# Performance work log

Measured on AMD Instinct MI355X. Metric: run time of the kernel, lower is better.

Reference implementation:

```python
import jax, jax.numpy as jnp
import numpy as np

NC, NU, K, C, P, O = 20, 16, 128, 2048, 5, 256

def setup_inputs() -> dict:
    key = jax.random.key(0)
    ks = jax.random.split(key, 6)
    s = 0.02  # keep activations well-scaled
    return {
        "topk_feats": jax.random.normal(ks[0], (NC, NU, K, C), jnp.float32),
        "prototypes": jax.random.normal(ks[1], (NC, P, C), jnp.float32),
        "w_inner1": jax.random.normal(ks[2], (O, C), jnp.float32) * s,
        "w_inner_trans": jax.random.normal(ks[3], (C, C), jnp.float32) * s,
        "w_inter1": jax.random.normal(ks[4], (O, C), jnp.float32) * s,
        "w_inter2": jax.random.normal(ks[5], (O, C), jnp.float32) * s,
    }

def reference(topk_feats, prototypes, w_inner1, w_inner_trans, w_inter1, w_inter2):
    scale = 1.0 / jnp.sqrt(jnp.asarray(O, topk_feats.dtype))
    # --- inner (per-group) self-attention, vmapped over (class, unlabel) ---
    # fe: [nc, nu, k, o]
    fe = jnp.einsum("nukc,oc->nuko", topk_feats, w_inner1)
    att = jax.nn.softmax(jnp.einsum("nuko,nulo->nukl", fe, fe) * scale, axis=-1)
    agg = jnp.einsum("nukl,nulc->nukc", att, topk_feats)  # atte @ feat
    feats = topk_feats + jax.nn.relu(jnp.einsum("nukc,dc->nukd", agg, w_inner_trans))
    # --- inter (prototype -> all feats) cross-attention per class ---
    fa = feats.reshape(NC, NU * K, C)  # cat over unlabel dim
    fae = jnp.einsum("nmc,oc->nmo", fa, w_inter1)
    pe = jnp.einsum("npc,oc->npo", prototypes, w_inter2)
    att2 = jax.nn.softmax(jnp.einsum("npo,nmo->npm", pe, fae) * scale, axis=-1)
    un_protos = jnp.einsum("npm,nmc->npc", att2, fa)  # [nc, p, c]
    return un_protos
```

## Files before the change

kernel.cpp:

```cpp
#include <hip/hip_runtime.h>

typedef __attribute__((ext_vector_type(4))) float f32x4;
typedef __attribute__((ext_vector_type(8))) short short8;

#define DEVI static __device__ __forceinline__

DEVI unsigned short f2bf(float f) {
  unsigned int u = __float_as_uint(f);
  u += 0x7FFFu + ((u >> 16) & 1u);
  return (unsigned short)(u >> 16);
}
DEVI float bf2f(unsigned short s) { return __uint_as_float(((unsigned int)s) << 16); }
DEVI unsigned int pack2(float lo, float hi) {
  return ((unsigned int)f2bf(hi) << 16) | (unsigned int)f2bf(lo);
}

#define GL2LDS(gp, lp)                                                        \
  __builtin_amdgcn_global_load_lds(                                           \
      (const __attribute__((address_space(1))) void*)(const void*)(gp),       \
      (__attribute__((address_space(3))) void*)(void*)(lp), 16, 0, 0)

__global__ __launch_bounds__(256) void k_cvt_bf16(const float* __restrict__ src,
                                                  unsigned short* __restrict__ dst, int n4) {
  int i = blockIdx.x * 256 + threadIdx.x;
  if (i < n4) {
    float4 v = ((const float4*)src)[i];
    uint2 o; o.x = pack2(v.x, v.y); o.y = pack2(v.z, v.w);
    ((uint2*)dst)[i] = o;
  }
}

template <bool RES>
__global__ __launch_bounds__(256) void k_gemm_bt(const unsigned short* __restrict__ A,
                                                 const unsigned short* __restrict__ B,
                                                 unsigned short* __restrict__ C,
                                                 const float* __restrict__ resid, int N) {
  constexpr int K = 2048;
  __shared__ unsigned short lA[128 * 64];
  __shared__ unsigned short lB[128 * 64];
  const int tid = threadIdx.x;
  const int lane = tid & 63;
  const int wave = tid >> 6;
  const int wr = wave >> 1, wc = wave & 1;
  const long mBase = (long)blockIdx.y * 128;
  const long nBase = (long)blockIdx.x * 128;

  f32x4 acc[4][4] = {};

  for (int k0 = 0; k0 < K; k0 += 64) {
    __syncthreads();
#pragma unroll
    for (int it = 0; it < 4; it++) {
      int idx = it * 256 + wave * 64 + lane;
      int row = idx >> 3;
      int kc = idx & 7;
      int skc = kc ^ (row & 7);
      const unsigned short* ga = A + (mBase + row) * (long)K + k0 + skc * 8;
      const unsigned short* gb = B + (nBase + row) * (long)K + k0 + skc * 8;
      int lbase = (it * 256 + wave * 64) * 8;
      GL2LDS(ga, &lA[lbase]);
      GL2LDS(gb, &lB[lbase]);
    }
    __syncthreads();
#pragma unroll
    for (int kb = 0; kb < 2; kb++) {
      short8 af[4], bfr[4];
#pragma unroll
      for (int mt = 0; mt < 4; mt++) {
        int row = wr * 64 + mt * 16 + (lane & 15);
        int slot = (kb * 4 + (lane >> 4)) ^ (row & 7);
        af[mt] = *(const short8*)&lA[row * 64 + slot * 8];
      }
#pragma unroll
      for (int nt = 0; nt < 4; nt++) {
        int row = wc * 64 + nt * 16 + (lane & 15);
        int slot = (kb * 4 + (lane >> 4)) ^ (row & 7);
        bfr[nt] = *(const short8*)&lB[row * 64 + slot * 8];
      }
#pragma unroll
      for (int mt = 0; mt < 4; mt++)
#pragma unroll
        for (int nt = 0; nt < 4; nt++)
          acc[mt][nt] = __builtin_amdgcn_mfma_f32_16x16x32_bf16(af[mt], bfr[nt], acc[mt][nt], 0, 0, 0);
    }
  }
#pragma unroll
  for (int mt = 0; mt < 4; mt++) {
#pragma unroll
    for (int nt = 0; nt < 4; nt++) {
#pragma unroll
      for (int j = 0; j < 4; j++) {
        long row = mBase + wr * 64 + mt * 16 + (lane >> 4) * 4 + j;
        long col = nBase + wc * 64 + nt * 16 + (lane & 15);
        float v = acc[mt][nt][j];
        if constexpr (RES) v = resid[row * (long)N + col] + fmaxf(v, 0.0f);
        C[row * (long)N + col] = f2bf(v);
      }
    }
  }
}

template <bool RES>
__global__ __launch_bounds__(512, 2) void k_gemm256(const unsigned short* __restrict__ A,
                                                    const unsigned short* __restrict__ B,
                                                    unsigned short* __restrict__ C,
                                                    const float* __restrict__ resid, int N) {
  constexpr int K = 2048;
  __shared__ unsigned short lA[2][256 * 64];
  __shared__ unsigned short lB[2][256 * 64];
  const int tid = threadIdx.x;
  const int lane = tid & 63;
  const int wave = tid >> 6;
  const int wr = wave >> 2, wc = wave & 3;
  const long mBase = (long)blockIdx.y * 256;
  const long nBase = (long)blockIdx.x * 256;

  f32x4 acc[8][4] = {};

  auto stage = [&](int buf, int k0) {
#pragma unroll
    for (int it = 0; it < 4; it++) {
      int idx = it * 512 + tid;
      int row = idx >> 3, kc = idx & 7;
      int skc = kc ^ (row & 7);
      int lbase = (it * 512 + (tid & ~63)) * 8;
      GL2LDS(A + (mBase + row) * (long)K + k0 + skc * 8, &lA[buf][lbase]);
      GL2LDS(B + (nBase + row) * (long)K + k0 + skc * 8, &lB[buf][lbase]);
    }
  };

  stage(0, 0);
  for (int t = 0; t < 32; t++) {
    const int cur = t & 1;
    if (t < 31) {
      stage(cur ^ 1, (t + 1) * 64);
      asm volatile("s_waitcnt vmcnt(8)" ::: "memory");
    } else {
      asm volatile("s_waitcnt vmcnt(0)" ::: "memory");
    }
    __builtin_amdgcn_s_barrier();
    __builtin_amdgcn_sched_barrier(0);
    const unsigned short* bA = &lA[cur][0];
    const unsigned short* bB = &lB[cur][0];
#pragma unroll
    for (int kb = 0; kb < 2; kb++) {
      short8 af[8], bfr[4];
#pragma unroll
      for (int mt = 0; mt < 8; mt++) {
        int row = wr * 128 + mt * 16 + (lane & 15);
        int slot = (kb * 4 + (lane >> 4)) ^ (row & 7);
        af[mt] = *(const short8*)&bA[row * 64 + slot * 8];
      }
#pragma unroll
      for (int nt = 0; nt < 4; nt++) {
        int row = wc * 64 + nt * 16 + (lane & 15);
        int slot = (kb * 4 + (lane >> 4)) ^ (row & 7);
        bfr[nt] = *(const short8*)&bB[row * 64 + slot * 8];
      }
#pragma unroll
      for (int mt = 0; mt < 8; mt++)
#pragma unroll
        for (int nt = 0; nt < 4; nt++)
          acc[mt][nt] = __builtin_amdgcn_mfma_f32_16x16x32_bf16(af[mt], bfr[nt], acc[mt][nt], 0, 0, 0);
    }
    __builtin_amdgcn_sched_barrier(0);
    __builtin_amdgcn_s_barrier();
  }
#pragma unroll
  for (int mt = 0; mt < 8; mt++) {
#pragma unroll
    for (int nt = 0; nt < 4; nt++) {
#pragma unroll
      for (int j = 0; j < 4; j++) {
        long row = mBase + wr * 128 + mt * 16 + (lane >> 4) * 4 + j;
        long col = nBase + wc * 64 + nt * 16 + (lane & 15);
        float v = acc[mt][nt][j];
        if constexpr (RES) v = resid[row * (long)N + col] + fmaxf(v, 0.0f);
        C[row * (long)N + col] = f2bf(v);
      }
    }
  }
}

__global__ __launch_bounds__(256) void k_attn_inner(const unsigned short* __restrict__ fe,
                                                    const unsigned short* __restrict__ topkb,
                                                    unsigned short* __restrict__ agg) {
  __shared__ unsigned short attb[128 * 136];
  __shared__ unsigned short featT[64 * 128];
  __shared__ float redmax[2 * 128];
  __shared__ float redsum[2 * 128];
  const int tid = threadIdx.x;
  const int lane = tid & 63;
  const int wave = tid >> 6;
  const int wr = wave >> 1, wc = wave & 1;
  const int g = blockIdx.x;
  const unsigned short* feG = fe + (long)g * 128 * 256;

  f32x4 s[4][4] = {};
#pragma unroll
  for (int kb = 0; kb < 8; kb++) {
    short8 af[4], bfr[4];
#pragma unroll
    for (int mt = 0; mt < 4; mt++) {
      int row = wr * 64 + mt * 16 + (lane & 15);
      af[mt] = *(const short8*)(feG + row * 256 + kb * 32 + (lane >> 4) * 8);
    }
#pragma unroll
    for (int nt = 0; nt < 4; nt++) {
      int row = wc * 64 + nt * 16 + (lane & 15);
      bfr[nt] = *(const short8*)(feG + row * 256 + kb * 32 + (lane >> 4) * 8);
    }
#pragma unroll
    for (int mt = 0; mt < 4; mt++)
#pragma unroll
      for (int nt = 0; nt < 4; nt++)
        s[mt][nt] = __builtin_amdgcn_mfma_f32_16x16x32_bf16(af[mt], bfr[nt], s[mt][nt], 0, 0, 0);
  }

  const float cexp = 0.0625f * 1.44269504088896f;
#pragma unroll
  for (int mt = 0; mt < 4; mt++) {
#pragma unroll
    for (int j = 0; j < 4; j++) {
      float m = fmaxf(fmaxf(s[mt][0][j], s[mt][1][j]), fmaxf(s[mt][2][j], s[mt][3][j]));
#pragma unroll
      for (int d = 1; d < 16; d <<= 1) m = fmaxf(m, __shfl_xor(m, d, 64));
      int r = wr * 64 + mt * 16 + (lane >> 4) * 4 + j;
      if ((lane & 15) == 0) redmax[wc * 128 + r] = m;
    }
  }
  __syncthreads();
#pragma unroll
  for (int mt = 0; mt < 4; mt++) {
#pragma unroll
    for (int j = 0; j < 4; j++) {
      int r = wr * 64 + mt * 16 + (lane >> 4) * 4 + j;
      float M = fmaxf(redmax[r], redmax[128 + r]);
      float sm = 0.f;
#pragma unroll
      for (int nt = 0; nt < 4; nt++) {
        float p = exp2f((s[mt][nt][j] - M) * cexp);
        s[mt][nt][j] = p;
        sm += p;
      }
#pragma unroll
      for (int d = 1; d < 16; d <<= 1) sm += __shfl_xor(sm, d, 64);
      if ((lane & 15) == 0) redsum[wc * 128 + r] = sm;
    }
  }
  __syncthreads();
#pragma unroll
  for (int mt = 0; mt < 4; mt++) {
#pragma unroll
    for (int j = 0; j < 4; j++) {
      int r = wr * 64 + mt * 16 + (lane >> 4) * 4 + j;
      float inv = 1.0f / (redsum[r] + redsum[128 + r]);
#pragma unroll
      for (int nt = 0; nt < 4; nt++) {
        int c = wc * 64 + nt * 16 + (lane & 15);
        attb[r * 136 + c] = f2bf(s[mt][nt][j] * inv);
      }
    }
  }

  for (int ch = 0; ch < 32; ch++) {
    __syncthreads();
#pragma unroll
    for (int i = 0; i < 4; i++) {
      int seg = i * 256 + tid;
      int l = seg >> 3, kc = seg & 7;
      const unsigned short* gp = topkb + ((long)g * 128 + l) * 2048 + ch * 64 + kc * 8;
      uint4 w = *(const uint4*)gp;
      unsigned short v[8];
      v[0] = (unsigned short)(w.x & 0xffff); v[1] = (unsigned short)(w.x >> 16);
      v[2] = (unsigned short)(w.y & 0xffff); v[3] = (unsigned short)(w.y >> 16);
      v[4] = (unsigned short)(w.z & 0xffff); v[5] = (unsigned short)(w.z >> 16);
      v[6] = (unsigned short)(w.w & 0xffff); v[7] = (unsigned short)(w.w >> 16);
      int lx = l ^ (kc << 3);
#pragma unroll
      for (int j = 0; j < 8; j++) featT[(kc * 8 + j) * 128 + lx] = v[j];
    }
    __syncthreads();
    f32x4 c[2][4] = {};
#pragma unroll
    for (int kb = 0; kb < 4; kb++) {
      short8 af2[2], bf2v[4];
#pragma unroll
      for (int mt = 0; mt < 2; mt++) {
        int r = wave * 32 + mt * 16 + (lane & 15);
        af2[mt] = *(const short8*)&attb[r * 136 + kb * 32 + (lane >> 4) * 8];
      }
#pragma unroll
      for (int nt = 0; nt < 4; nt++) {
        int cc = nt * 16 + (lane & 15);
        int l0 = (kb * 32 + (lane >> 4) * 8) ^ (((cc >> 3) & 7) << 3);
        bf2v[nt] = *(const short8*)&featT[cc * 128 + l0];
      }
#pragma unroll
      for (int mt = 0; mt < 2; mt++)
#pragma unroll
        for (int nt = 0; nt < 4; nt++)
          c[mt][nt] = __builtin_amdgcn_mfma_f32_16x16x32_bf16(af2[mt], bf2v[nt], c[mt][nt], 0, 0, 0);
    }
#pragma unroll
    for (int mt = 0; mt < 2; mt++)
#pragma unroll
      for (int nt = 0; nt < 4; nt++)
#pragma unroll
        for (int j = 0; j < 4; j++) {
          long row = (long)g * 128 + wave * 32 + mt * 16 + (lane >> 4) * 4 + j;
          int col = ch * 64 + nt * 16 + (lane & 15);
          agg[row * 2048 + col] = f2bf(c[mt][nt][j]);
        }
  }
}

__global__ __launch_bounds__(256) void k_pe(const float* __restrict__ protos,
                                            const float* __restrict__ wi2,
                                            float* __restrict__ pe) {
  int n = blockIdx.x, oc = blockIdx.y, tid = threadIdx.x;
  if (tid < 160) {
    int p = tid >> 5, o = oc * 32 + (tid & 31);
    const float* pr = protos + ((long)n * 5 + p) * 2048;
    const float* wr = wi2 + (long)o * 2048;
    float acc = 0.f;
    for (int cidx = 0; cidx < 2048; cidx += 4) {
      float4 a = *(const float4*)(pr + cidx);
      float4 b = *(const float4*)(wr + cidx);
      acc += a.x * b.x + a.y * b.y + a.z * b.z + a.w * b.w;
    }
    pe[((long)n * 5 + p) * 256 + o] = acc;
  }
}

__global__ __launch_bounds__(256) void k_q(const float* __restrict__ pe,
                                           const float* __restrict__ wi1,
                                           float* __restrict__ q) {
  __shared__ float pel[1280];
  int n = blockIdx.x, cb = blockIdx.y, tid = threadIdx.x;
  for (int i = tid; i < 1280; i += 256) pel[i] = pe[(long)n * 1280 + i];
  __syncthreads();
  int c = cb * 256 + tid;
  float a[5] = {0.f, 0.f, 0.f, 0.f, 0.f};
  for (int o = 0; o < 256; o++) {
    float w = wi1[(long)o * 2048 + c];
#pragma unroll
    for (int p = 0; p < 5; p++) a[p] += pel[p * 256 + o] * w;
  }
#pragma unroll
  for (int p = 0; p < 5; p++) q[((long)n * 5 + p) * 2048 + c] = a[p];
}

__global__ __launch_bounds__(256) void k_lg(const float* __restrict__ q,
                                            const unsigned short* __restrict__ feats,
                                            float* __restrict__ lg) {
  __shared__ float ql[5 * 2048];
  int n = blockIdx.x, mc = blockIdx.y, tid = threadIdx.x;
  const float* qs = q + (long)n * 5 * 2048;
  for (int i = tid; i < 2560; i += 256) ((float4*)ql)[i] = ((const float4*)qs)[i];
  __syncthreads();
  int m = mc * 256 + tid;
  const unsigned short* fr = feats + ((long)n * 2048 + m) * 2048;
  float a[5] = {0.f, 0.f, 0.f, 0.f, 0.f};
  for (int c = 0; c < 2048; c += 8) {
    uint4 w = *(const uint4*)(fr + c);
    float f[8];
    f[0] = bf2f((unsigned short)(w.x & 0xffff)); f[1] = bf2f((unsigned short)(w.x >> 16));
    f[2] = bf2f((unsigned short)(w.y & 0xffff)); f[3] = bf2f((unsigned short)(w.y >> 16));
    f[4] = bf2f((unsigned short)(w.z & 0xffff)); f[5] = bf2f((unsigned short)(w.z >> 16));
    f[6] = bf2f((unsigned short)(w.w & 0xffff)); f[7] = bf2f((unsigned short)(w.w >> 16));
#pragma unroll
    for (int j = 0; j < 8; j++) {
      float fv = f[j];
#pragma unroll
      for (int p = 0; p < 5; p++) a[p] += fv * ql[p * 2048 + c + j];
    }
  }
#pragma unroll
  for (int p = 0; p < 5; p++) lg[((long)n * 5 + p) * 2048 + m] = a[p] * 0.0625f;
}

__global__ __launch_bounds__(256) void k_sm(const float* __restrict__ lg,
                                            float* __restrict__ att2) {
  __shared__ float red[4], red2[4];
  int b = blockIdx.x, tid = threadIdx.x;
  const float* src = lg + (long)b * 2048;
  float v[8];
  float mx = -1e30f;
#pragma unroll
  for (int i = 0; i < 8; i++) { v[i] = src[i * 256 + tid]; mx = fmaxf(mx, v[i]); }
#pragma unroll
  for (int d = 1; d < 64; d <<= 1) mx = fmaxf(mx, __shfl_xor(mx, d, 64));
  if ((tid & 63) == 0) red[tid >> 6] = mx;
  __syncthreads();
  mx = fmaxf(fmaxf(red[0], red[1]), fmaxf(red[2], red[3]));
  float sm = 0.f;
#pragma unroll
  for (int i = 0; i < 8; i++) { v[i] = exp2f((v[i] - mx) * 1.44269504088896f); sm += v[i]; }
#pragma unroll
  for (int d = 1; d < 64; d <<= 1) sm += __shfl_xor(sm, d, 64);
  if ((tid & 63) == 0) red2[tid >> 6] = sm;
  __syncthreads();
  float inv = 1.0f / (red2[0] + red2[1] + red2[2] + red2[3]);
  float* dst = att2 + (long)b * 2048;
#pragma unroll
  for (int i = 0; i < 8; i++) dst[i * 256 + tid] = v[i] * inv;
}

__global__ __launch_bounds__(256) void k_out_part(const float* __restrict__ att2,
                                                  const unsigned short* __restrict__ feats,
                                                  float* __restrict__ partial) {
  __shared__ float a2[5 * 512];
  int n = blockIdx.x, cb = blockIdx.y, ms = blockIdx.z;
  int tid = threadIdx.x;
  const float* src = att2 + (long)n * 5 * 2048 + ms * 512;
  for (int i = tid; i < 640; i += 256) {
    int p = i >> 7, qq = i & 127;
    ((float4*)a2)[i] = *(const float4*)(src + p * 2048 + qq * 4);
  }
  __syncthreads();
  int c0 = cb * 1024 + tid * 4;
  const unsigned short* fp = feats + ((long)n * 2048 + ms * 512) * 2048 + c0;
  float acc[5][4] = {};
  for (int m = 0; m < 512; m++) {
    uint2 w = *(const uint2*)(fp + (long)m * 2048);
    float f0 = bf2f((unsigned short)(w.x & 0xffff));
    float f1 = bf2f((unsigned short)(w.x >> 16));
    float f2 = bf2f((unsigned short)(w.y & 0xffff));
    float f3 = bf2f((unsigned short)(w.y >> 16));
#pragma unroll
    for (int p = 0; p < 5; p++) {
      float a = a2[p * 512 + m];
      acc[p][0] += a * f0; acc[p][1] += a * f1; acc[p][2] += a * f2; acc[p][3] += a * f3;
    }
  }
  float* pp = partial + ((long)ms * 100 + (long)n * 5) * 2048;
#pragma unroll
  for (int p = 0; p < 5; p++) {
    float4 o; o.x = acc[p][0]; o.y = acc[p][1]; o.z = acc[p][2]; o.w = acc[p][3];
    *(float4*)(pp + p * 2048 + c0) = o;
  }
}

__global__ __launch_bounds__(256) void k_out_red(const float* __restrict__ partial,
                                                 float* __restrict__ outp) {
  int i = blockIdx.x * 256 + threadIdx.x;
  const f32x4* P = (const f32x4*)partial;
  f32x4 s = P[i] + P[51200 + i] + P[2 * 51200 + i] + P[3 * 51200 + i];
  ((f32x4*)outp)[i] = s;
}

extern "C" void kernel_launch(void* const* d_in, const int* in_sizes, int n_in,
                              void* d_out, int out_size, void* d_ws, size_t ws_size,
                              hipStream_t stream) {
  const float* topk = (const float*)d_in[0];
  const float* protos = (const float*)d_in[1];
  const float* w1 = (const float*)d_in[2];
  const float* wt = (const float*)d_in[3];
  const float* wi1 = (const float*)d_in[4];
  const float* wi2 = (const float*)d_in[5];
  float* outp = (float*)d_out;

  char* ws = (char*)d_ws;
  size_t off = 0;
  auto alloc = [&](size_t bytes) -> void* {
    void* p = ws + off;
    off += (bytes + 255) & ~(size_t)255;
    return p;
  };
  unsigned short* w1b = (unsigned short*)alloc((size_t)256 * 2048 * 2);
  unsigned short* wtb = (unsigned short*)alloc((size_t)2048 * 2048 * 2);
  unsigned short* topkb = (unsigned short*)alloc((size_t)40960 * 2048 * 2);
  unsigned short* fe = (unsigned short*)alloc((size_t)40960 * 256 * 2);
  unsigned short* agg = (unsigned short*)alloc((size_t)40960 * 2048 * 2);
  float* pe = (float*)alloc((size_t)20 * 5 * 256 * 4);
  float* q = (float*)alloc((size_t)20 * 5 * 2048 * 4);
  float* lg = (float*)alloc((size_t)20 * 5 * 2048 * 4);
  float* att2 = (float*)alloc((size_t)20 * 5 * 2048 * 4);
  float* partial = (float*)alloc((size_t)4 * 20 * 5 * 2048 * 4);
  unsigned short* feats = topkb;

  k_cvt_bf16<<<512, 256, 0, stream>>>(w1, w1b, 131072);
  k_cvt_bf16<<<4096, 256, 0, stream>>>(wt, wtb, 1048576);
  k_cvt_bf16<<<81920, 256, 0, stream>>>(topk, topkb, 20971520);

  k_gemm_bt<false><<<dim3(2, 320), 256, 0, stream>>>(topkb, w1b, fe, nullptr, 256);
  k_attn_inner<<<320, 256, 0, stream>>>(fe, topkb, agg);
  k_gemm256<true><<<dim3(8, 160), 512, 0, stream>>>(agg, wtb, feats, topk, 2048);
  k_pe<<<dim3(20, 8), 256, 0, stream>>>(protos, wi2, pe);
  k_q<<<dim3(20, 8), 256, 0, stream>>>(pe, wi1, q);
  k_lg<<<dim3(20, 8), 256, 0, stream>>>(q, feats, lg);
  k_sm<<<100, 256, 0, stream>>>(lg, att2);
  k_out_part<<<dim3(20, 2, 4), 256, 0, stream>>>(att2, feats, partial);
  k_out_red<<<200, 256, 0, stream>>>(partial, outp);
}
```

Measured before the change: 1.041 ms.

## Double-buffer small GEMM, swizzle block order, split tail kernels for more parallelism

The 128-tile GEMM gets double-buffered LDS staging with explicit vmcnt waits so loads overlap MFMA work. Both GEMMs also remap block indices in an XCD-aware swizzle to improve L2 locality. The logits kernel is split along channels into two partial outputs that the softmax kernel sums, and the output kernel uses narrower per-thread column chunks with twice as many blocks. The aim is to raise occupancy in the tail kernels, which launch too few blocks to fill the GPU. The cost is more LDS, extra partial buffers and slightly more memory traffic.

```diff
diff --git a/kernel.cpp b/kernel.cpp
--- a/kernel.cpp
+++ b/kernel.cpp
@@ -36,32 +36,46 @@
                                                  unsigned short* __restrict__ C,
                                                  const float* __restrict__ resid, int N) {
   constexpr int K = 2048;
-  __shared__ unsigned short lA[128 * 64];
-  __shared__ unsigned short lB[128 * 64];
+  __shared__ unsigned short lA[2][128 * 64];
+  __shared__ unsigned short lB[2][128 * 64];
   const int tid = threadIdx.x;
   const int lane = tid & 63;
   const int wave = tid >> 6;
   const int wr = wave >> 1, wc = wave & 1;
-  const long mBase = (long)blockIdx.y * 128;
-  const long nBase = (long)blockIdx.x * 128;
+  const int nx = gridDim.x;
+  const int lin = blockIdx.y * nx + blockIdx.x;
+  const int cpx = (nx * gridDim.y) >> 3;
+  const int swz = (lin & 7) * cpx + (lin >> 3);
+  const long mBase = (long)(swz / nx) * 128;
+  const long nBase = (long)(swz % nx) * 128;
 
   f32x4 acc[4][4] = {};
 
-  for (int k0 = 0; k0 < K; k0 += 64) {
-    __syncthreads();
+  auto stage = [&](int buf, int k0) {
 #pragma unroll
     for (int it = 0; it < 4; it++) {
-      int idx = it * 256 + wave * 64 + lane;
-      int row = idx >> 3;
-      int kc = idx & 7;
+      int idx = it * 256 + tid;
+      int row = idx >> 3, kc = idx & 7;
       int skc = kc ^ (row & 7);
-      const unsigned short* ga = A + (mBase + row) * (long)K + k0 + skc * 8;
-      const unsigned short* gb = B + (nBase + row) * (long)K + k0 + skc * 8;
-      int lbase = (it * 256 + wave * 64) * 8;
-      GL2LDS(ga, &lA[lbase]);
-      GL2LDS(gb, &lB[lbase]);
-    }
-    __syncthreads();
+      int lbase = (it * 256 + (tid & ~63)) * 8;
+      GL2LDS(A + (mBase + row) * (long)K + k0 + skc * 8, &lA[buf][lbase]);
+      GL2LDS(B + (nBase + row) * (long)K + k0 + skc * 8, &lB[buf][lbase]);
+    }
+  };
+
+  stage(0, 0);
+  for (int t = 0; t < 32; t++) {
+    const int cur = t & 1;
+    if (t < 31) {
+      stage(cur ^ 1, (t + 1) * 64);
+      asm volatile("s_waitcnt vmcnt(8)" ::: "memory");
+    } else {
+      asm volatile("s_waitcnt vmcnt(0)" ::: "memory");
+    }
+    __builtin_amdgcn_s_barrier();
+    __builtin_amdgcn_sched_barrier(0);
+    const unsigned short* bA = &lA[cur][0];
+    const unsigned short* bB = &lB[cur][0];
 #pragma unroll
     for (int kb = 0; kb < 2; kb++) {
       short8 af[4], bfr[4];
@@ -69,13 +83,13 @@
       for (int mt = 0; mt < 4; mt++) {
         int row = wr * 64 + mt * 16 + (lane & 15);
         int slot = (kb * 4 + (lane >> 4)) ^ (row & 7);
-        af[mt] = *(const short8*)&lA[row * 64 + slot * 8];
+        af[mt] = *(const short8*)&bA[row * 64 + slot * 8];
       }
 #pragma unroll
       for (int nt = 0; nt < 4; nt++) {
         int row = wc * 64 + nt * 16 + (lane & 15);
         int slot = (kb * 4 + (lane >> 4)) ^ (row & 7);
-        bfr[nt] = *(const short8*)&lB[row * 64 + slot * 8];
+        bfr[nt] = *(const short8*)&bB[row * 64 + slot * 8];
       }
 #pragma unroll
       for (int mt = 0; mt < 4; mt++)
@@ -83,6 +97,8 @@
         for (int nt = 0; nt < 4; nt++)
           acc[mt][nt] = __builtin_amdgcn_mfma_f32_16x16x32_bf16(af[mt], bfr[nt], acc[mt][nt], 0, 0, 0);
     }
+    __builtin_amdgcn_sched_barrier(0);
+    __builtin_amdgcn_s_barrier();
   }
 #pragma unroll
   for (int mt = 0; mt < 4; mt++) {
@@ -112,8 +128,10 @@
   const int lane = tid & 63;
   const int wave = tid >> 6;
   const int wr = wave >> 2, wc = wave & 3;
-  const long mBase = (long)blockIdx.y * 256;
-  const long nBase = (long)blockIdx.x * 256;
+  const int lin = blockIdx.y * 8 + blockIdx.x;
+  const int swz = (lin & 7) * 160 + (lin >> 3);
+  const long mBase = (long)(swz >> 3) * 256;
+  const long nBase = (long)(swz & 7) * 256;
 
   f32x4 acc[8][4] = {};
 
@@ -353,16 +371,19 @@
 
 __global__ __launch_bounds__(256) void k_lg(const float* __restrict__ q,
                                             const unsigned short* __restrict__ feats,
-                                            float* __restrict__ lg) {
-  __shared__ float ql[5 * 2048];
-  int n = blockIdx.x, mc = blockIdx.y, tid = threadIdx.x;
-  const float* qs = q + (long)n * 5 * 2048;
-  for (int i = tid; i < 2560; i += 256) ((float4*)ql)[i] = ((const float4*)qs)[i];
+                                            float* __restrict__ lgp) {
+  __shared__ float ql[5 * 1024];
+  int n = blockIdx.x, mc = blockIdx.y, cb = blockIdx.z, tid = threadIdx.x;
+  const float4* qs = (const float4*)(q + (long)n * 5 * 2048);
+  for (int i = tid; i < 1280; i += 256) {
+    int p = i >> 8, r = i & 255;
+    ((float4*)ql)[i] = qs[p * 512 + cb * 256 + r];
+  }
   __syncthreads();
   int m = mc * 256 + tid;
-  const unsigned short* fr = feats + ((long)n * 2048 + m) * 2048;
+  const unsigned short* fr = feats + ((long)n * 2048 + m) * 2048 + cb * 1024;
   float a[5] = {0.f, 0.f, 0.f, 0.f, 0.f};
-  for (int c = 0; c < 2048; c += 8) {
+  for (int c = 0; c < 1024; c += 8) {
     uint4 w = *(const uint4*)(fr + c);
     float f[8];
     f[0] = bf2f((unsigned short)(w.x & 0xffff)); f[1] = bf2f((unsigned short)(w.x >> 16));
@@ -373,22 +394,27 @@
     for (int j = 0; j < 8; j++) {
       float fv = f[j];
 #pragma unroll
-      for (int p = 0; p < 5; p++) a[p] += fv * ql[p * 2048 + c + j];
-    }
-  }
-#pragma unroll
-  for (int p = 0; p < 5; p++) lg[((long)n * 5 + p) * 2048 + m] = a[p] * 0.0625f;
-}
-
-__global__ __launch_bounds__(256) void k_sm(const float* __restrict__ lg,
+      for (int p = 0; p < 5; p++) a[p] += fv * ql[p * 1024 + c + j];
+    }
+  }
+#pragma unroll
+  for (int p = 0; p < 5; p++)
+    lgp[((long)cb * 100 + n * 5 + p) * 2048 + m] = a[p] * 0.0625f;
+}
+
+__global__ __launch_bounds__(256) void k_sm(const float* __restrict__ lgp,
                                             float* __restrict__ att2) {
   __shared__ float red[4], red2[4];
   int b = blockIdx.x, tid = threadIdx.x;
-  const float* src = lg + (long)b * 2048;
+  const float* s0 = lgp + (long)b * 2048;
+  const float* s1 = lgp + (long)100 * 2048 + (long)b * 2048;
   float v[8];
   float mx = -1e30f;
 #pragma unroll
-  for (int i = 0; i < 8; i++) { v[i] = src[i * 256 + tid]; mx = fmaxf(mx, v[i]); }
+  for (int i = 0; i < 8; i++) {
+    v[i] = s0[i * 256 + tid] + s1[i * 256 + tid];
+    mx = fmaxf(mx, v[i]);
+  }
 #pragma unroll
   for (int d = 1; d < 64; d <<= 1) mx = fmaxf(mx, __shfl_xor(mx, d, 64));
   if ((tid & 63) == 0) red[tid >> 6] = mx;
@@ -419,26 +445,25 @@
     ((float4*)a2)[i] = *(const float4*)(src + p * 2048 + qq * 4);
   }
   __syncthreads();
-  int c0 = cb * 1024 + tid * 4;
+  int c0 = cb * 512 + tid * 2;
   const unsigned short* fp = feats + ((long)n * 2048 + ms * 512) * 2048 + c0;
-  float acc[5][4] = {};
+  float acc[5][2] = {};
   for (int m = 0; m < 512; m++) {
-    uint2 w = *(const uint2*)(fp + (long)m * 2048);
-    float f0 = bf2f((unsigned short)(w.x & 0xffff));
-    float f1 = bf2f((unsigned short)(w.x >> 16));
-    float f2 = bf2f((unsigned short)(w.y & 0xffff));
-    float f3 = bf2f((unsigned short)(w.y >> 16));
+    unsigned int w = *(const unsigned int*)(fp + (long)m * 2048);
+    float f0 = bf2f((unsigned short)(w & 0xffff));
+    float f1 = bf2f((unsigned short)(w >> 16));
 #pragma unroll
     for (int p = 0; p < 5; p++) {
       float a = a2[p * 512 + m];
-      acc[p][0] += a * f0; acc[p][1] += a * f1; acc[p][2] += a * f2; acc[p][3] += a * f3;
+      acc[p][0] += a * f0;
+      acc[p][1] += a * f1;
     }
   }
   float* pp = partial + ((long)ms * 100 + (long)n * 5) * 2048;
 #pragma unroll
   for (int p = 0; p < 5; p++) {
-    float4 o; o.x = acc[p][0]; o.y = acc[p][1]; o.z = acc[p][2]; o.w = acc[p][3];
-    *(float4*)(pp + p * 2048 + c0) = o;
+    float2 o; o.x = acc[p][0]; o.y = acc[p][1];
+    *(float2*)(pp + p * 2048 + c0) = o;
   }
 }
 
@@ -475,9 +500,9 @@
   unsigned short* agg = (unsigned short*)alloc((size_t)40960 * 2048 * 2);
   float* pe = (float*)alloc((size_t)20 * 5 * 256 * 4);
   float* q = (float*)alloc((size_t)20 * 5 * 2048 * 4);
-  float* lg = (float*)alloc((size_t)20 * 5 * 2048 * 4);
+  float* lgp = (float*)alloc((size_t)2 * 100 * 2048 * 4);
   float* att2 = (float*)alloc((size_t)20 * 5 * 2048 * 4);
-  float* partial = (float*)alloc((size_t)4 * 20 * 5 * 2048 * 4);
+  float* partial = (float*)alloc((size_t)4 * 100 * 2048 * 4);
   unsigned short* feats = topkb;
 
   k_cvt_bf16<<<512, 256, 0, stream>>>(w1, w1b, 131072);
@@ -489,8 +514,8 @@
   k_gemm256<true><<<dim3(8, 160), 512, 0, stream>>>(agg, wtb, feats, topk, 2048);
   k_pe<<<dim3(20, 8), 256, 0, stream>>>(protos, wi2, pe);
   k_q<<<dim3(20, 8), 256, 0, stream>>>(pe, wi1, q);
-  k_lg<<<dim3(20, 8), 256, 0, stream>>>(q, feats, lg);
-  k_sm<<<100, 256, 0, stream>>>(lg, att2);
-  k_out_part<<<dim3(20, 2, 4), 256, 0, stream>>>(att2, feats, partial);
+  k_lg<<<dim3(20, 8, 2), 256, 0, stream>>>(q, feats, lgp);
+  k_sm<<<100, 256, 0, stream>>>(lgp, att2);
+  k_out_part<<<dim3(20, 4, 4), 256, 0, stream>>>(att2, feats, partial);
   k_out_red<<<200, 256, 0, stream>>>(partial, outp);
 }
```

Measured after the change: 982.2 us. -5.7%, faster.
